# Optimization experiments

Hardware: AMD Instinct MI355X
Metric: run time of the kernel (lower is better)

## Reference

```python
import jax, jax.numpy as jnp
import numpy as np

N_NODES = 50000
N_EDGES = 800000
NODE_DIM = 3
EDGE_DIM = 32
HIDDEN = 128
NUM_GRAPHS = 256


def _linear_init(key, fan_in, fan_out):
    # torch nn.Linear default: U(-1/sqrt(fan_in), 1/sqrt(fan_in))
    kw, kb = jax.random.split(key)
    bound = 1.0 / np.sqrt(fan_in)
    W = jax.random.uniform(kw, (fan_in, fan_out), jnp.float32, -bound, bound)
    b = jax.random.uniform(kb, (fan_out,), jnp.float32, -bound, bound)
    return W, b


def setup_inputs() -> dict:
    key = jax.random.key(0)
    ks = jax.random.split(key, 16)
    x = jax.random.normal(ks[0], (N_NODES, NODE_DIM), jnp.float32)
    edge_index = jax.random.randint(ks[1], (2, N_EDGES), 0, N_NODES, jnp.int64)
    edge_attr = jax.random.uniform(ks[2], (N_EDGES, EDGE_DIM), jnp.float32)
    batch = jnp.sort(jax.random.randint(ks[3], (N_NODES,), 0, NUM_GRAPHS, jnp.int64))

    # conv1: CGConv(channels=3, dim=32) -> lin_f, lin_s: (2*3+32) -> 3
    Wf1, bf1 = _linear_init(ks[4], 2 * NODE_DIM + EDGE_DIM, NODE_DIM)
    Ws1, bs1 = _linear_init(ks[5], 2 * NODE_DIM + EDGE_DIM, NODE_DIM)
    # node_proj: 3 -> 128
    Wp, bp = _linear_init(ks[6], NODE_DIM, HIDDEN)
    zin = 2 * HIDDEN + EDGE_DIM
    Wf_list, bf_list, Ws_list, bs_list = [], [], [], []
    for i in range(2):
        Wf, bf = _linear_init(ks[7 + i], zin, HIDDEN)
        Ws, bs = _linear_init(ks[9 + i], zin, HIDDEN)
        Wf_list.append(Wf); bf_list.append(bf); Ws_list.append(Ws); bs_list.append(bs)
    Wf_convs = jnp.stack(Wf_list); bf_convs = jnp.stack(bf_list)
    Ws_convs = jnp.stack(Ws_list); bs_convs = jnp.stack(bs_list)
    # fc1: 128 -> 128
    W1, b1 = _linear_init(ks[11], HIDDEN, HIDDEN)
    # 5 heads: 128 -> 1, stacked as (5, 128) and (5,)
    Wh_list, bh_list = [], []
    for i in range(5):
        Wh, bh = _linear_init(jax.random.fold_in(ks[12], i), HIDDEN, 1)
        Wh_list.append(Wh[:, 0]); bh_list.append(bh[0])
    W_heads = jnp.stack(Wh_list)  # (5, 128)
    b_heads = jnp.stack(bh_list)  # (5,)

    return dict(x=x, edge_index=edge_index, edge_attr=edge_attr, batch=batch,
                Wf1=Wf1, bf1=bf1, Ws1=Ws1, bs1=bs1, Wp=Wp, bp=bp,
                Wf_convs=Wf_convs, bf_convs=bf_convs, Ws_convs=Ws_convs, bs_convs=bs_convs,
                W1=W1, b1=b1, W_heads=W_heads, b_heads=b_heads)


def _cgconv(x, src, dst, edge_attr, Wf, bf, Ws, bs):
    # PyG CGConv: z_ij = [x_i || x_j || e_ij], messages aggregated to i (dst)
    z = jnp.concatenate([x[dst], x[src], edge_attr], axis=-1)  # [E, 2C+D]
    msg = jax.nn.sigmoid(z @ Wf + bf) * jax.nn.softplus(z @ Ws + bs)  # [E, C]
    agg = jax.ops.segment_sum(msg, dst, num_segments=x.shape[0])
    return x + agg


def reference(x, edge_index, edge_attr, batch,
              Wf1, bf1, Ws1, bs1, Wp, bp,
              Wf_convs, bf_convs, Ws_convs, bs_convs,
              W1, b1, W_heads, b_heads):
    src, dst = edge_index[0], edge_index[1]
    h = _cgconv(x, src, dst, edge_attr, Wf1, bf1, Ws1, bs1)
    h = jax.nn.relu(h @ Wp + bp)
    for l in range(Wf_convs.shape[0]):
        h = _cgconv(h, src, dst, edge_attr, Wf_convs[l], bf_convs[l], Ws_convs[l], bs_convs[l])
        h = jax.nn.relu(h)
    # global mean pool over graphs
    sums = jax.ops.segment_sum(h, batch, num_segments=NUM_GRAPHS)
    counts = jax.ops.segment_sum(jnp.ones((h.shape[0],), h.dtype), batch, num_segments=NUM_GRAPHS)
    g = sums / jnp.maximum(counts, 1.0)[:, None]  # [G, H]
    g = jax.nn.relu(g @ W1 + b1)
    # 5 heads stacked -> [G, 5] (columns: volume, band_gap, formation_energy, density, bulk_modulus)
    out = g @ W_heads.T + b_heads
    return out
```

## Files before the change

### kernel.cpp

```cpp
#include <hip/hip_runtime.h>
#include <hip/hip_bf16.h>
#include <math.h>

#define N_NODES 50000
#define N_EDGES 800000
#define NODE_DIM 3
#define EDGE_DIM 32
#define HIDDEN 128
#define NUM_GRAPHS 256
#define ZIN (2*HIDDEN + EDGE_DIM)
#define NPAD 50176

#define LOG2E 1.44269504088896f
#define LN2   0.69314718055995f

typedef __attribute__((ext_vector_type(8))) short short8;
typedef __attribute__((ext_vector_type(4))) float f32x4;

__device__ __forceinline__ unsigned short f2bf(float x) {
    unsigned u = __float_as_uint(x);
    u += 0x7FFFu + ((u >> 16) & 1u);
    return (unsigned short)(u >> 16);
}
__device__ __forceinline__ float bf_lo(unsigned u) { return __uint_as_float(u << 16); }
__device__ __forceinline__ float bf_hi(unsigned u) { return __uint_as_float(u & 0xFFFF0000u); }

__global__ __launch_bounds__(256) void conv1_sorted_kernel(
    const float* __restrict__ x, const float* __restrict__ EA,
    const int4* __restrict__ epack,
    const float* __restrict__ Wf1, const float* __restrict__ bf1,
    const float* __restrict__ Ws1, const float* __restrict__ bs1,
    float* __restrict__ agg0)
{
    __shared__ float WfL[38*3], WsL[38*3], bfL[3], bsL[3];
    __shared__ float msgL[256*4];
    __shared__ int   pdL[256];

    if (threadIdx.x < 114) {
        WfL[threadIdx.x] = Wf1[threadIdx.x] * LOG2E;
        WsL[threadIdx.x] = Ws1[threadIdx.x] * LOG2E;
    }
    if (threadIdx.x < 3) {
        bfL[threadIdx.x] = bf1[threadIdx.x] * LOG2E;
        bsL[threadIdx.x] = bs1[threadIdx.x] * LOG2E;
    }
    __syncthreads();

    const int p = blockIdx.x * 256 + threadIdx.x;
    int4 e = epack[p];
    const int eid = e.x, s = e.y, d = e.z;
    pdL[threadIdx.x] = d;

    float z[38];
    z[0] = x[d*3+0]; z[1] = x[d*3+1]; z[2] = x[d*3+2];
    z[3] = x[s*3+0]; z[4] = x[s*3+1]; z[5] = x[s*3+2];
    const float4* ep = (const float4*)(EA + (size_t)eid * EDGE_DIM);
    #pragma unroll
    for (int q = 0; q < 8; ++q) {
        float4 v = ep[q];
        z[6+4*q+0] = v.x; z[6+4*q+1] = v.y; z[6+4*q+2] = v.z; z[6+4*q+3] = v.w;
    }
    float f[3], g[3];
    #pragma unroll
    for (int c = 0; c < 3; ++c) { f[c] = bfL[c]; g[c] = bsL[c]; }
    #pragma unroll
    for (int j = 0; j < 38; ++j) {
        #pragma unroll
        for (int c = 0; c < 3; ++c) {
            f[c] += z[j] * WfL[j*3+c];
            g[c] += z[j] * WsL[j*3+c];
        }
    }
    #pragma unroll
    for (int c = 0; c < 3; ++c) {
        float sig = __builtin_amdgcn_rcpf(1.0f + __builtin_amdgcn_exp2f(-f[c]));
        float sp  = fmaxf(g[c], 0.0f) + __builtin_amdgcn_logf(1.0f + __builtin_amdgcn_exp2f(-fabsf(g[c])));
        msgL[threadIdx.x*4 + c] = sig * sp;
    }
    __syncthreads();

    if (threadIdx.x < 48) {
        const int c   = threadIdx.x % 3;
        const int seg = threadIdx.x / 3;
        const int base = seg * 16;
        float acc = 0.0f;
        int cur = pdL[base];
        #pragma unroll 4
        for (int i = 0; i < 16; ++i) {
            int dd = pdL[base + i];
            float v = msgL[(base + i)*4 + c];
            if (dd != cur) {
                atomicAdd(agg0 + (size_t)cur*3 + c, acc);
                acc = 0.0f; cur = dd;
            }
            acc += v;
        }
        atomicAdd(agg0 + (size_t)cur*3 + c, acc);
    }
}

__global__ __launch_bounds__(256) void proj_kernel(
    const float* __restrict__ x, const float* __restrict__ agg0,
    const float* __restrict__ Wp, const float* __restrict__ bp,
    float* __restrict__ H)
{
    int idx = blockIdx.x * 256 + threadIdx.x;
    if (idx >= N_NODES * HIDDEN) return;
    int n = idx >> 7, c = idx & 127;
    float h0 = fmaf(agg0[n*3+0], LN2, x[n*3+0]);
    float h1 = fmaf(agg0[n*3+1], LN2, x[n*3+1]);
    float h2 = fmaf(agg0[n*3+2], LN2, x[n*3+2]);
    float v = bp[c] + h0*Wp[0*128+c] + h1*Wp[1*128+c] + h2*Wp[2*128+c];
    H[idx] = fmaxf(v, 0.0f);
}

__global__ __launch_bounds__(256) void hist_kernel(
    const int* __restrict__ ei, int* __restrict__ hist)
{
    int e = blockIdx.x * 256 + threadIdx.x;
    if (e < N_EDGES) atomicAdd(&hist[ei[N_EDGES + e]], 1);
}

__global__ __launch_bounds__(256) void scanA_kernel(
    const int* __restrict__ hist, int* __restrict__ cursor, int* __restrict__ btot)
{
    __shared__ int tmp[256];
    int t = threadIdx.x;
    int i = blockIdx.x * 256 + t;
    int v = hist[i];
    tmp[t] = v;
    __syncthreads();
    #pragma unroll
    for (int off = 1; off < 256; off <<= 1) {
        int y = (t >= off) ? tmp[t - off] : 0;
        __syncthreads();
        if (t >= off) tmp[t] += y;
        __syncthreads();
    }
    cursor[i] = tmp[t] - v;
    if (t == 255) btot[blockIdx.x] = tmp[t];
}

__global__ __launch_bounds__(256) void scanB_kernel(int* __restrict__ btot)
{
    __shared__ int tmp[256];
    int t = threadIdx.x;
    int v = btot[t];
    tmp[t] = v;
    __syncthreads();
    #pragma unroll
    for (int off = 1; off < 256; off <<= 1) {
        int y = (t >= off) ? tmp[t - off] : 0;
        __syncthreads();
        if (t >= off) tmp[t] += y;
        __syncthreads();
    }
    btot[t] = tmp[t] - v;
}

__global__ __launch_bounds__(256) void scanC_kernel(
    int* __restrict__ cursor, const int* __restrict__ btot)
{
    int i = blockIdx.x * 256 + threadIdx.x;
    cursor[i] += btot[blockIdx.x];
}

__global__ __launch_bounds__(256) void scatter_kernel(
    const int* __restrict__ ei, int* __restrict__ cursor,
    int4* __restrict__ epack)
{
    int e = blockIdx.x * 256 + threadIdx.x;
    if (e >= N_EDGES) return;
    int s = ei[e];
    int d = ei[N_EDGES + e];
    int p = atomicAdd(&cursor[d], 1);
    epack[p] = make_int4(e, s, d, 0);
}

__global__ __launch_bounds__(256) void repack_frag_kernel(
    const float* __restrict__ Wf, const float* __restrict__ Ws,
    unsigned short* __restrict__ Bfrag)
{
    int idx = blockIdx.x * 256 + threadIdx.x;
    if (idx >= 2*32*4*64) return;
    int lane = idx & 63;
    int kc   = (idx >> 6) & 3;
    int nt   = (idx >> 8) & 31;
    int l    = idx >> 13;
    const float* wf  = Wf + (size_t)l * ZIN * HIDDEN;
    const float* wsp = Ws + (size_t)l * ZIN * HIDDEN;
    int n = nt*16 + (lane & 15);
    int half = n >> 8;
    int within = n & 255;
    int cc = within >> 1;
    int t = within & 1;
    const float* W = t ? wsp : wf;
    unsigned short vals[8];
    #pragma unroll
    for (int j = 0; j < 8; ++j) {
        int k = kc*32 + (lane >> 4)*8 + j;
        vals[j] = f2bf(W[(size_t)(half*128 + k)*128 + cc] * LOG2E);
    }
    *(short8*)(Bfrag + (size_t)idx * 8) = *(short8*)vals;
}

__global__ __launch_bounds__(256) void repack_edge_frag_kernel(
    const float* __restrict__ Wf, const float* __restrict__ Ws,
    unsigned short* __restrict__ BE)
{
    int idx = blockIdx.x * 256 + threadIdx.x;
    if (idx >= 2*16*64) return;
    int lane = idx & 63;
    int nt   = (idx >> 6) & 15;
    int l    = idx >> 10;
    const float* W = ((nt & 8) ? Ws : Wf) + (size_t)l * ZIN * HIDDEN + 256*128;
    int c = (nt & 7)*16 + (lane & 15);
    unsigned short vals[8];
    #pragma unroll
    for (int j = 0; j < 8; ++j) {
        int k = (lane >> 4)*8 + j;
        vals[j] = f2bf(W[(size_t)k*128 + c] * LOG2E);
    }
    *(short8*)(BE + (size_t)idx * 8) = *(short8*)vals;
}

__global__ __launch_bounds__(256) void gemm_mfma(
    const float* __restrict__ H, const float* __restrict__ aggIn,
    const unsigned short* __restrict__ Bfrag,
    const float* __restrict__ bf, const float* __restrict__ bs,
    unsigned short* __restrict__ Pb)
{
    const int lane = threadIdx.x & 63;
    const int wave = threadIdx.x >> 6;
    const int m    = lane & 15;
    const int quad = lane >> 4;
    const int rowA = blockIdx.y * 64 + wave * 16 + m;
    const int colBase = blockIdx.x * 256;

    const float* hrow = H + (size_t)rowA * 128;
    short8 a[4];
    #pragma unroll
    for (int kc = 0; kc < 4; ++kc) {
        float4 v0 = *(const float4*)(hrow + kc*32 + quad*8);
        float4 v1 = *(const float4*)(hrow + kc*32 + quad*8 + 4);
        if (aggIn) {
            const float* arow = aggIn + (size_t)rowA * 128;
            float4 a0 = *(const float4*)(arow + kc*32 + quad*8);
            float4 a1 = *(const float4*)(arow + kc*32 + quad*8 + 4);
        v0.x = fmaxf(fmaf(a0.x, LN2, v0.x), 0.f); v0.y = fmaxf(fmaf(a0.y, LN2, v0.y), 0.f);
        v0.z = fmaxf(fmaf(a0.z, LN2, v0.z), 0.f); v0.w = fmaxf(fmaf(a0.w, LN2, v0.w), 0.f);
        v1.x = fmaxf(fmaf(a1.x, LN2, v1.x), 0.f); v1.y = fmaxf(fmaf(a1.y, LN2, v1.y), 0.f);
        v1.z = fmaxf(fmaf(a1.z, LN2, v1.z), 0.f); v1.w = fmaxf(fmaf(a1.w, LN2, v1.w), 0.f);
        }
        unsigned short t[8];
        t[0]=f2bf(v0.x); t[1]=f2bf(v0.y); t[2]=f2bf(v0.z); t[3]=f2bf(v0.w);
        t[4]=f2bf(v1.x); t[5]=f2bf(v1.y); t[6]=f2bf(v1.z); t[7]=f2bf(v1.w);
        a[kc] = *(short8*)t;
    }

    f32x4 acc[16];
    #pragma unroll
    for (int nt = 0; nt < 16; ++nt) {
        float bias = 0.0f;
        if (colBase == 0) {
            int col = nt*16 + m;
            bias = ((col & 1) ? bs[col >> 1] : bf[col >> 1]) * LOG2E;
        }
        acc[nt] = (f32x4){bias, bias, bias, bias};
    }

    #pragma unroll
    for (int nt = 0; nt < 16; ++nt) {
        int ntg = (colBase >> 4) + nt;
        const unsigned short* bp = Bfrag + ((size_t)(ntg*4) * 64 + lane) * 8;
        #pragma unroll
        for (int kc = 0; kc < 4; ++kc) {
            short8 b = *(const short8*)(bp + (size_t)kc * 64 * 8);
            acc[nt] = __builtin_amdgcn_mfma_f32_16x16x32_bf16(a[kc], b, acc[nt], 0, 0, 0);
        }
    }

    const int rowC = blockIdx.y * 64 + wave * 16 + quad * 4;
    #pragma unroll
    for (int nt = 0; nt < 16; ++nt) {
        int col = colBase + nt*16 + m;
        #pragma unroll
        for (int r = 0; r < 4; ++r) {
            int row = rowC + r;
            if (row < N_NODES) Pb[(size_t)row * 512 + col] = f2bf(acc[nt][r]);
        }
    }
}

__global__ __launch_bounds__(256) void edge_kernel(
    const unsigned short* __restrict__ Pb, const float* __restrict__ EA,
    const int4* __restrict__ epack,
    const unsigned short* __restrict__ BE,
    float* __restrict__ agg)
{
    __shared__ float msgL[64*132];
    __shared__ int pdL[64];
    __shared__ unsigned bmask[2];

    if (threadIdx.x < 64) {
        const int t = threadIdx.x;
        int d = epack[blockIdx.x*64 + t].z;
        pdL[t] = d;
        bool b = (t & 31) ? (d != pdL[t-1]) : false;
        unsigned long long bal = __ballot(b);
        if (t == 0) { bmask[0] = (unsigned)bal; bmask[1] = (unsigned)(bal >> 32); }
    }

    const int lane = threadIdx.x & 63;
    const int wave = threadIdx.x >> 6;
    const int m    = lane & 15;
    const int quad = lane >> 4;
    const int p0   = blockIdx.x * 64 + wave * 16;

    int eid = epack[p0 + m].x;
    const float* ea = EA + (size_t)eid * EDGE_DIM + quad*8;
    float4 v0 = *(const float4*)ea;
    float4 v1 = *(const float4*)(ea + 4);
    unsigned short t[8];
    t[0]=f2bf(v0.x); t[1]=f2bf(v0.y); t[2]=f2bf(v0.z); t[3]=f2bf(v0.w);
    t[4]=f2bf(v1.x); t[5]=f2bf(v1.y); t[6]=f2bf(v1.z); t[7]=f2bf(v1.w);
    short8 a = *(short8*)t;

    const unsigned short* pdp[4];
    const unsigned short* psp[4];
    float* mrow[4];
    #pragma unroll
    for (int r = 0; r < 4; ++r) {
        int4 e = epack[p0 + quad*4 + r];
        pdp[r] = Pb + (size_t)e.z * 512 + 2*m;
        psp[r] = Pb + (size_t)e.y * 512 + 256 + 2*m;
        mrow[r] = &msgL[(wave*16 + quad*4 + r)*132 + m];
    }

    const short8* BEv = (const short8*)BE;
    const f32x4 zero = (f32x4){0.f, 0.f, 0.f, 0.f};
    #pragma unroll
    for (int nt = 0; nt < 8; ++nt) {
        short8 bF = BEv[nt*64 + lane];
        short8 bS = BEv[(nt+8)*64 + lane];
        f32x4 qf = __builtin_amdgcn_mfma_f32_16x16x32_bf16(a, bF, zero, 0, 0, 0);
        f32x4 qs = __builtin_amdgcn_mfma_f32_16x16x32_bf16(a, bS, zero, 0, 0, 0);
        #pragma unroll
        for (int r = 0; r < 4; ++r) {
            unsigned pd = *(const unsigned*)(pdp[r] + nt*32);
            unsigned ps = *(const unsigned*)(psp[r] + nt*32);
            float f = bf_lo(pd) + bf_lo(ps) + qf[r];
            float g = bf_hi(pd) + bf_hi(ps) + qs[r];
            float sig = __builtin_amdgcn_rcpf(1.0f + __builtin_amdgcn_exp2f(-f));
            float sp  = fmaxf(g, 0.0f) + __builtin_amdgcn_logf(1.0f + __builtin_amdgcn_exp2f(-fabsf(g)));
            mrow[r][nt*16] = sig * sp;
        }
    }
    __syncthreads();

    const int c2  = threadIdx.x & 127;
    const int seg = threadIdx.x >> 7;
    const int base = seg * 32;
    unsigned msk = bmask[seg];
    const float* mcol = &msgL[base*132 + c2];
    float acc = 0.0f;
    #pragma unroll 4
    for (int i = 0; i < 32; ++i) {
        float v = mcol[i*132];
        if (msk & 1u) {
            atomicAdd(&agg[(size_t)pdL[base + i - 1] * HIDDEN + c2], acc);
            acc = 0.0f;
        }
        msk >>= 1;
        acc += v;
    }
    atomicAdd(&agg[(size_t)pdL[base + 31] * HIDDEN + c2], acc);
}

__global__ __launch_bounds__(128) void pool_kernel(
    const float* __restrict__ H, const float* __restrict__ agg1,
    const float* __restrict__ agg2, const int* __restrict__ batch,
    float* __restrict__ gsum, float* __restrict__ gcnt)
{
    const int c = threadIdx.x;
    const int n0 = blockIdx.x * 128;
    float acc = 0.0f;
    int cur = -1;
    for (int i = 0; i < 128; ++i) {
        int n = n0 + i;
        if (n >= N_NODES) break;
        int g = batch[n];
        if (g != cur) {
            if (cur >= 0) atomicAdd(gsum + (size_t)cur * HIDDEN + c, acc);
            cur = g; acc = 0.0f;
        }
        size_t ix = (size_t)n * HIDDEN + c;
        float h = fmaxf(fmaf(agg2[ix], LN2, fmaxf(fmaf(agg1[ix], LN2, H[ix]), 0.0f)), 0.0f);
        acc += h;
    }
    if (cur >= 0) atomicAdd(gsum + (size_t)cur * HIDDEN + c, acc);

    if (c == 0) {
        int curg = -1; float run = 0.0f;
        for (int i = 0; i < 128; ++i) {
            int n = n0 + i;
            if (n >= N_NODES) break;
            int g = batch[n];
            if (g != curg) {
                if (curg >= 0) atomicAdd(gcnt + curg, run);
                curg = g; run = 0.0f;
            }
            run += 1.0f;
        }
        if (curg >= 0) atomicAdd(gcnt + curg, run);
    }
}

__global__ __launch_bounds__(128) void head_kernel(
    const float* __restrict__ gsum, const float* __restrict__ gcnt,
    const float* __restrict__ W1, const float* __restrict__ b1,
    const float* __restrict__ Wh, const float* __restrict__ bh,
    float* __restrict__ out)
{
    __shared__ float gavg[128];
    __shared__ float g1[128];
    const int g = blockIdx.x, c = threadIdx.x;
    float cnt = fmaxf(gcnt[g], 1.0f);
    gavg[c] = gsum[(size_t)g * HIDDEN + c] / cnt;
    __syncthreads();
    float acc = b1[c];
    for (int k = 0; k < 128; ++k) acc += gavg[k] * W1[k*128 + c];
    g1[c] = fmaxf(acc, 0.0f);
    __syncthreads();
    if (c < 5) {
        float o = bh[c];
        for (int k = 0; k < 128; ++k) o += g1[k] * Wh[c*128 + k];
        out[(size_t)g * 5 + c] = o;
    }
}

extern "C" void kernel_launch(void* const* d_in, const int* in_sizes, int n_in,
                              void* d_out, int out_size, void* d_ws, size_t ws_size,
                              hipStream_t stream) {
    const float* x        = (const float*)d_in[0];
    const int*   ei       = (const int*)  d_in[1];
    const float* EA       = (const float*)d_in[2];
    const int*   batch    = (const int*)  d_in[3];
    const float* Wf1      = (const float*)d_in[4];
    const float* bf1      = (const float*)d_in[5];
    const float* Ws1      = (const float*)d_in[6];
    const float* bs1      = (const float*)d_in[7];
    const float* Wp       = (const float*)d_in[8];
    const float* bp       = (const float*)d_in[9];
    const float* Wf_convs = (const float*)d_in[10];
    const float* bf_convs = (const float*)d_in[11];
    const float* Ws_convs = (const float*)d_in[12];
    const float* bs_convs = (const float*)d_in[13];
    const float* W1       = (const float*)d_in[14];
    const float* b1       = (const float*)d_in[15];
    const float* W_heads  = (const float*)d_in[16];
    const float* b_heads  = (const float*)d_in[17];
    float* out = (float*)d_out;

    float* ws = (float*)d_ws;
    float* agg0 = ws + 0;
    float* H    = ws + 150016;
    unsigned short* Pb = (unsigned short*)(ws + 6550016);
    float* agg1 = ws + 19350016;
    float* agg2 = ws + 25750016;
    unsigned short* Bfrag = (unsigned short*)(ws + 32150016);
    unsigned short* BE    = (unsigned short*)(ws + 32215552);
    float* gsum = ws + 32223744;
    float* gcnt = ws + 32256512;
    int* hist   = (int*)(ws + 32257024);
    int* cursor = (int*)(ws + 32307200);
    int* btot   = (int*)(ws + 32357376);
    int4* epack = (int4*)(ws + 32357632);

    hipMemsetAsync(hist, 0, (size_t)(2*NPAD + 256) * sizeof(int), stream);
    hist_kernel<<<(N_EDGES + 255)/256, 256, 0, stream>>>(ei, hist);
    scanA_kernel<<<NPAD/256, 256, 0, stream>>>(hist, cursor, btot);
    scanB_kernel<<<1, 256, 0, stream>>>(btot);
    scanC_kernel<<<NPAD/256, 256, 0, stream>>>(cursor, btot);
    scatter_kernel<<<(N_EDGES + 255)/256, 256, 0, stream>>>(ei, cursor, epack);

    hipMemsetAsync(agg0, 0, (size_t)N_NODES * 3 * sizeof(float), stream);
    conv1_sorted_kernel<<<N_EDGES/256, 256, 0, stream>>>(x, EA, epack, Wf1, bf1, Ws1, bs1, agg0);
    proj_kernel<<<(N_NODES*HIDDEN + 255)/256, 256, 0, stream>>>(x, agg0, Wp, bp, H);
    repack_frag_kernel<<<(2*32*4*64 + 255)/256, 256, 0, stream>>>(Wf_convs, Ws_convs, Bfrag);
    repack_edge_frag_kernel<<<(2*16*64 + 255)/256, 256, 0, stream>>>(Wf_convs, Ws_convs, BE);

    dim3 ggrid(2, (N_NODES + 63)/64);
    gemm_mfma<<<ggrid, 256, 0, stream>>>(H, nullptr, Bfrag, bf_convs, bs_convs, Pb);
    hipMemsetAsync(agg1, 0, (size_t)N_NODES * HIDDEN * sizeof(float), stream);
    edge_kernel<<<N_EDGES/64, 256, 0, stream>>>(Pb, EA, epack, BE, agg1);
    gemm_mfma<<<ggrid, 256, 0, stream>>>(H, agg1, Bfrag + (size_t)32*4*64*8,
                                         bf_convs + HIDDEN, bs_convs + HIDDEN, Pb);
    hipMemsetAsync(agg2, 0, (size_t)N_NODES * HIDDEN * sizeof(float), stream);
    edge_kernel<<<N_EDGES/64, 256, 0, stream>>>(Pb, EA, epack, BE + (size_t)16*64*8, agg2);

    hipMemsetAsync(gsum, 0, (size_t)(NUM_GRAPHS * HIDDEN + NUM_GRAPHS) * sizeof(float), stream);
    pool_kernel<<<(N_NODES + 127)/128, 128, 0, stream>>>(H, agg1, agg2, batch, gsum, gcnt);
    head_kernel<<<NUM_GRAPHS, 128, 0, stream>>>(gsum, gcnt, W1, b1, W_heads, b_heads, out);
}
```

Before: 662.1 us.

## Transpose and swizzle edge message staging, fold gathered sums into MFMA accumulator

The edge kernel now stages messages in shared memory transposed (channel-major) with an XOR-style chunk swizzle, written as float4 and read back as float4 in the segmented reduction, so bank conflicts and scalar LDS traffic drop. The gathered dst/src projections are passed as the MFMA accumulator input instead of being added afterward, which removes separate adds. The boundary mask is read via readfirstlane so it stays in a scalar register. The two agg memsets are merged into one earlier call, which assumes agg2 sits directly after agg1 in the workspace.

Result: no change. 653.7 us (-1.3%).

```diff
diff --git a/kernel.cpp b/kernel.cpp
--- a/kernel.cpp
+++ b/kernel.cpp
@@ -298,9 +298,9 @@
     const unsigned short* __restrict__ BE,
     float* __restrict__ agg)
 {
-    __shared__ float msgL[64*132];
+    __shared__ float msgL[128*68];
     __shared__ int pdL[64];
-    __shared__ unsigned bmask[2];
+    __shared__ unsigned bmaskL[2];
 
     if (threadIdx.x < 64) {
         const int t = threadIdx.x;
@@ -308,7 +308,7 @@
         pdL[t] = d;
         bool b = (t & 31) ? (d != pdL[t-1]) : false;
         unsigned long long bal = __ballot(b);
-        if (t == 0) { bmask[0] = (unsigned)bal; bmask[1] = (unsigned)(bal >> 32); }
+        if (t == 0) { bmaskL[0] = (unsigned)bal; bmaskL[1] = (unsigned)(bal >> 32); }
     }
 
     const int lane = threadIdx.x & 63;
@@ -328,53 +328,65 @@
 
     const unsigned short* pdp[4];
     const unsigned short* psp[4];
-    float* mrow[4];
     #pragma unroll
     for (int r = 0; r < 4; ++r) {
         int4 e = epack[p0 + quad*4 + r];
         pdp[r] = Pb + (size_t)e.z * 512 + 2*m;
         psp[r] = Pb + (size_t)e.y * 512 + 256 + 2*m;
-        mrow[r] = &msgL[(wave*16 + quad*4 + r)*132 + m];
     }
 
     const short8* BEv = (const short8*)BE;
-    const f32x4 zero = (f32x4){0.f, 0.f, 0.f, 0.f};
+    const int chunk  = wave*4 + quad;
     #pragma unroll
     for (int nt = 0; nt < 8; ++nt) {
         short8 bF = BEv[nt*64 + lane];
         short8 bS = BEv[(nt+8)*64 + lane];
-        f32x4 qf = __builtin_amdgcn_mfma_f32_16x16x32_bf16(a, bF, zero, 0, 0, 0);
-        f32x4 qs = __builtin_amdgcn_mfma_f32_16x16x32_bf16(a, bS, zero, 0, 0, 0);
+        f32x4 accF, accS;
         #pragma unroll
         for (int r = 0; r < 4; ++r) {
             unsigned pd = *(const unsigned*)(pdp[r] + nt*32);
             unsigned ps = *(const unsigned*)(psp[r] + nt*32);
-            float f = bf_lo(pd) + bf_lo(ps) + qf[r];
-            float g = bf_hi(pd) + bf_hi(ps) + qs[r];
+            accF[r] = bf_lo(pd) + bf_lo(ps);
+            accS[r] = bf_hi(pd) + bf_hi(ps);
+        }
+        f32x4 qf = __builtin_amdgcn_mfma_f32_16x16x32_bf16(a, bF, accF, 0, 0, 0);
+        f32x4 qs = __builtin_amdgcn_mfma_f32_16x16x32_bf16(a, bS, accS, 0, 0, 0);
+        float4 mv;
+        #pragma unroll
+        for (int r = 0; r < 4; ++r) {
+            float f = qf[r];
+            float g = qs[r];
             float sig = __builtin_amdgcn_rcpf(1.0f + __builtin_amdgcn_exp2f(-f));
             float sp  = fmaxf(g, 0.0f) + __builtin_amdgcn_logf(1.0f + __builtin_amdgcn_exp2f(-fabsf(g)));
-            mrow[r][nt*16] = sig * sp;
-        }
+            ((float*)&mv)[r] = sig * sp;
+        }
+        const int c = nt*16 + m;
+        const int chunkp = (chunk + 2*m) & 15;
+        *(float4*)&msgL[c*68 + chunkp*4] = mv;
     }
     __syncthreads();
 
     const int c2  = threadIdx.x & 127;
     const int seg = threadIdx.x >> 7;
-    const int base = seg * 32;
-    unsigned msk = bmask[seg];
-    const float* mcol = &msgL[base*132 + c2];
+    unsigned msk = (unsigned)__builtin_amdgcn_readfirstlane((int)bmaskL[seg]);
+    const int swz = 2*(c2 & 15);
+    const float* row = &msgL[c2*68];
     float acc = 0.0f;
-    #pragma unroll 4
-    for (int i = 0; i < 32; ++i) {
-        float v = mcol[i*132];
-        if (msk & 1u) {
-            atomicAdd(&agg[(size_t)pdL[base + i - 1] * HIDDEN + c2], acc);
-            acc = 0.0f;
-        }
-        msk >>= 1;
-        acc += v;
-    }
-    atomicAdd(&agg[(size_t)pdL[base + 31] * HIDDEN + c2], acc);
+    #pragma unroll
+    for (int jj = 0; jj < 8; ++jj) {
+        const int ch = seg*8 + jj;
+        const float4 v4 = *(const float4*)&row[((ch + swz) & 15)*4];
+        #pragma unroll
+        for (int k = 0; k < 4; ++k) {
+            if (msk & 1u) {
+                atomicAdd(&agg[(size_t)pdL[ch*4 + k - 1] * HIDDEN + c2], acc);
+                acc = 0.0f;
+            }
+            msk >>= 1;
+            acc += ((const float*)&v4)[k];
+        }
+    }
+    atomicAdd(&agg[(size_t)pdL[seg*32 + 31] * HIDDEN + c2], acc);
 }
 
 __global__ __launch_bounds__(128) void pool_kernel(
@@ -490,13 +502,13 @@
     repack_frag_kernel<<<(2*32*4*64 + 255)/256, 256, 0, stream>>>(Wf_convs, Ws_convs, Bfrag);
     repack_edge_frag_kernel<<<(2*16*64 + 255)/256, 256, 0, stream>>>(Wf_convs, Ws_convs, BE);
 
+    hipMemsetAsync(agg1, 0, (size_t)2 * N_NODES * HIDDEN * sizeof(float), stream);
+
     dim3 ggrid(2, (N_NODES + 63)/64);
     gemm_mfma<<<ggrid, 256, 0, stream>>>(H, nullptr, Bfrag, bf_convs, bs_convs, Pb);
-    hipMemsetAsync(agg1, 0, (size_t)N_NODES * HIDDEN * sizeof(float), stream);
     edge_kernel<<<N_EDGES/64, 256, 0, stream>>>(Pb, EA, epack, BE, agg1);
     gemm_mfma<<<ggrid, 256, 0, stream>>>(H, agg1, Bfrag + (size_t)32*4*64*8,
                                          bf_convs + HIDDEN, bs_convs + HIDDEN, Pb);
-    hipMemsetAsync(agg2, 0, (size_t)N_NODES * HIDDEN * sizeof(float), stream);
     edge_kernel<<<N_EDGES/64, 256, 0, stream>>>(Pb, EA, epack, BE + (size_t)16*64*8, agg2);
 
     hipMemsetAsync(gsum, 0, (size_t)(NUM_GRAPHS * HIDDEN + NUM_GRAPHS) * sizeof(float), stream);
```
